# Kernel tuning notes

Measured on AMD Instinct MI355X. Metric: run time of the kernel, lower is better.

## Reference

```python
import jax, jax.numpy as jnp
import numpy as np

B, T, D = 4, 2048, 1024
H = 16
HD = D // H  # 64


def setup_inputs() -> dict:
    key = jax.random.key(0)
    ks = jax.random.split(key, 5)
    scale = 0.02
    x = jax.random.normal(ks[0], (B, T, D), dtype=jnp.float32)
    W_qkv = jax.random.normal(ks[1], (D, 3 * D), dtype=jnp.float32) * scale
    b_qkv = jnp.zeros((3 * D,), dtype=jnp.float32)
    W_proj = jax.random.normal(ks[2], (D, D), dtype=jnp.float32) * scale
    b_proj = jnp.zeros((D,), dtype=jnp.float32)
    return {"x": x, "W_qkv": W_qkv, "b_qkv": b_qkv, "W_proj": W_proj, "b_proj": b_proj}


def reference(x, W_qkv, b_qkv, W_proj, b_proj):
    b, t, c = x.shape
    qkv = x @ W_qkv + b_qkv  # [b, t, 3c]
    q, k, v = jnp.split(qkv, 3, axis=-1)
    # [b, h, t, hd]
    q = q.reshape(b, t, H, HD).transpose(0, 2, 1, 3)
    k = k.reshape(b, t, H, HD).transpose(0, 2, 1, 3)
    v = v.reshape(b, t, H, HD).transpose(0, 2, 1, 3)
    att = jnp.einsum('bhqd,bhkd->bhqk', q, k) / jnp.sqrt(jnp.float32(HD))
    causal = jnp.tril(jnp.ones((t, t), dtype=bool))
    att = jnp.where(causal[None, None], att, jnp.float32(-jnp.inf))
    att = jax.nn.softmax(att, axis=-1)
    y = jnp.einsum('bhqk,bhkd->bhqd', att, v)
    y = y.transpose(0, 2, 1, 3).reshape(b, t, c)
    return y @ W_proj + b_proj
```

## Files before the change

### kernel.cpp

```cpp
#include <hip/hip_runtime.h>
#include <hip/hip_bf16.h>
#include <cmath>
#include <cstdint>

#define B_ 4
#define T_ 2048
#define D_ 1024
#define H_ 16
#define HD_ 64
#define M_ (B_*T_)
#define NQKV_ 3072

#define SCALE_Q 0.18033688011112042f

typedef float f32x4 __attribute__((ext_vector_type(4)));
typedef float f32x16 __attribute__((ext_vector_type(16)));
typedef __bf16 bf16x8 __attribute__((ext_vector_type(8)));
typedef __bf16 bf16x4 __attribute__((ext_vector_type(4)));

#define MFMA16(a, b, c) __builtin_amdgcn_mfma_f32_16x16x32_bf16((a), (b), (c), 0, 0, 0)
#define MFMA32(a, b, c) __builtin_amdgcn_mfma_f32_32x32x16_bf16((a), (b), (c), 0, 0, 0)

#if defined(__has_builtin)
#if __has_builtin(__builtin_amdgcn_global_load_lds)
#define HAVE_GLDS 1
#endif
#endif

#ifdef HAVE_GLDS
#define GLDS16(g, l) __builtin_amdgcn_global_load_lds( \
    (const __attribute__((address_space(1))) void*)(g), \
    (__attribute__((address_space(3))) void*)(l), 16, 0, 0)
#endif

__device__ inline float hexp2(float x) {
  float r; asm("v_exp_f32 %0, %1" : "=v"(r) : "v"(x)); return r;
}

__device__ inline uint32_t pack2bf(float a, float b) {
  union { __bf16 h[2]; uint32_t u; } x;
  x.h[0] = (__bf16)a; x.h[1] = (__bf16)b;
  return x.u;
}

__global__ __launch_bounds__(256) void k_cvt_bf16(const float4* __restrict__ in,
                                                  bf16x4* __restrict__ out, int n4) {
  int i = blockIdx.x * 256 + threadIdx.x;
  if (i >= n4) return;
  float4 v = in[i];
  bf16x4 o;
  o[0] = (__bf16)v.x; o[1] = (__bf16)v.y; o[2] = (__bf16)v.z; o[3] = (__bf16)v.w;
  out[i] = o;
}

__global__ __launch_bounds__(256) void k_transpose_cvt(const float* __restrict__ in,
                                                       __bf16* __restrict__ out,
                                                       int R, int C) {
  __shared__ float tile[64][65];
  int r0 = blockIdx.y * 64, c0 = blockIdx.x * 64;
#pragma unroll
  for (int i = 0; i < 16; ++i) {
    int e = threadIdx.x + i * 256;
    int lr = e >> 6, lc = e & 63;
    tile[lr][lc] = in[(size_t)(r0 + lr) * C + c0 + lc];
  }
  __syncthreads();
#pragma unroll
  for (int i = 0; i < 16; ++i) {
    int e = threadIdx.x + i * 256;
    int lc = e >> 6, lr = e & 63;
    out[(size_t)(c0 + lc) * R + r0 + lr] = (__bf16)tile[lr][lc];
  }
}

__global__ __launch_bounds__(512) void k_gemm256(const __bf16* __restrict__ A,
                                                 const __bf16* __restrict__ Bt,
                                                 const float* __restrict__ bias,
                                                 __bf16* __restrict__ Qb,
                                                 __bf16* __restrict__ Kb,
                                                 __bf16* __restrict__ Vtmp) {
  __shared__ __bf16 lA[256 * 32];
  __shared__ __bf16 lB[128 * 32];
  const int tid = threadIdx.x;
  const int lane = tid & 63, w = tid >> 6;
  const int wr = w >> 1, wc = w & 1;
  const int r15 = lane & 15, rg = lane >> 4;
  const int mb = blockIdx.y, nb = blockIdx.x;
  const int K = D_;
  const int nk = K >> 5;

  const f32x4 zero = {0.f, 0.f, 0.f, 0.f};
  f32x4 acc[4][4];
#pragma unroll
  for (int m = 0; m < 4; ++m)
#pragma unroll
    for (int n = 0; n < 4; ++n) acc[m][n] = zero;

  const int cA0 = tid, cA1 = tid + 512;
  const int rowA0 = cA0 >> 2, rowA1 = cA1 >> 2, offA = (tid & 3) * 8;
  const int rowB = tid >> 2;
  const __bf16* Ab = A + (size_t)(mb * 256) * K;
  const __bf16* Bb = Bt + (size_t)(nb * 128) * K;

  for (int kb = 0; kb < nk; ++kb) {
    __syncthreads();
#ifdef HAVE_GLDS
    GLDS16(Ab + (size_t)rowA0 * K + kb * 32 + offA, &lA[cA0 * 8]);
    GLDS16(Ab + (size_t)rowA1 * K + kb * 32 + offA, &lA[cA1 * 8]);
    GLDS16(Bb + (size_t)rowB * K + kb * 32 + offA, &lB[tid * 8]);
#else
    {
      bf16x8 ta0 = *(const bf16x8*)(Ab + (size_t)rowA0 * K + kb * 32 + offA);
      bf16x8 ta1 = *(const bf16x8*)(Ab + (size_t)rowA1 * K + kb * 32 + offA);
      bf16x8 tb0 = *(const bf16x8*)(Bb + (size_t)rowB * K + kb * 32 + offA);
      *(bf16x8*)(&lA[cA0 * 8]) = ta0;
      *(bf16x8*)(&lA[cA1 * 8]) = ta1;
      *(bf16x8*)(&lB[tid * 8]) = tb0;
    }
#endif
    __syncthreads();
    bf16x8 af[4], bfr[4];
#pragma unroll
    for (int m = 0; m < 4; ++m)
      af[m] = *(const bf16x8*)(&lA[(wr * 64 + m * 16 + r15) * 32 + rg * 8]);
#pragma unroll
    for (int n = 0; n < 4; ++n)
      bfr[n] = *(const bf16x8*)(&lB[(wc * 64 + n * 16 + r15) * 32 + rg * 8]);
#pragma unroll
    for (int m = 0; m < 4; ++m)
#pragma unroll
      for (int n = 0; n < 4; ++n)
        acc[m][n] = MFMA16(af[m], bfr[n], acc[m][n]);
  }

  const int row0 = mb * 256 + wr * 64;
  const int col0 = nb * 128 + wc * 64;
#pragma unroll
  for (int m = 0; m < 4; ++m) {
#pragma unroll
    for (int n = 0; n < 4; ++n) {
#pragma unroll
      for (int j = 0; j < 4; ++j) {
        int r = row0 + m * 16 + rg * 4 + j;
        int c = col0 + n * 16 + r15;
        float v = acc[m][n][j] + bias[c];
        int which = c >> 10, cc = c & 1023;
        int b = r >> 11, t = r & 2047;
        if (which == 0) {
          int hh = cc >> 6, hd = cc & 63;
          Qb[((size_t)(b * H_ + hh) * T_ + t) * HD_ + hd] = (__bf16)(v * SCALE_Q);
        } else if (which == 1) {
          int hh = cc >> 6, hd = cc & 63;
          Kb[((size_t)(b * H_ + hh) * T_ + t) * HD_ + hd] = (__bf16)v;
        } else {
          Vtmp[(size_t)r * D_ + cc] = (__bf16)v;
        }
      }
    }
  }
}

__global__ __launch_bounds__(256) void k_gemm_proj(const __bf16* __restrict__ A,
                                                   const __bf16* __restrict__ Bt,
                                                   const float* __restrict__ bias,
                                                   float* __restrict__ Cf,
                                                   int K, int N) {
  __shared__ __bf16 lA[128 * 32];
  __shared__ __bf16 lB[128 * 32];
  const int tid = threadIdx.x;
  const int lane = tid & 63, w = tid >> 6;
  const int wr = w >> 1, wc = w & 1;
  const int r15 = lane & 15, rg = lane >> 4;
  const int mb = blockIdx.y, nb = blockIdx.x;
  const int nk = K >> 5;

  const f32x4 zero = {0.f, 0.f, 0.f, 0.f};
  f32x4 acc[4][4];
#pragma unroll
  for (int m = 0; m < 4; ++m)
#pragma unroll
    for (int n = 0; n < 4; ++n) acc[m][n] = zero;

  const int c0 = tid, c1 = tid + 256;
  const int rowA0 = c0 >> 2, offA0 = (c0 & 3) * 8;
  const int rowA1 = c1 >> 2, offA1 = (c1 & 3) * 8;
  const __bf16* Ab = A + (size_t)(mb * 128) * K;
  const __bf16* Bb = Bt + (size_t)(nb * 128) * K;

  for (int kb = 0; kb < nk; ++kb) {
    __syncthreads();
#ifdef HAVE_GLDS
    GLDS16(Ab + (size_t)rowA0 * K + kb * 32 + offA0, &lA[c0 * 8]);
    GLDS16(Ab + (size_t)rowA1 * K + kb * 32 + offA1, &lA[c1 * 8]);
    GLDS16(Bb + (size_t)rowA0 * K + kb * 32 + offA0, &lB[c0 * 8]);
    GLDS16(Bb + (size_t)rowA1 * K + kb * 32 + offA1, &lB[c1 * 8]);
#else
    {
      bf16x8 ta0 = *(const bf16x8*)(Ab + (size_t)rowA0 * K + kb * 32 + offA0);
      bf16x8 ta1 = *(const bf16x8*)(Ab + (size_t)rowA1 * K + kb * 32 + offA1);
      bf16x8 tb0 = *(const bf16x8*)(Bb + (size_t)rowA0 * K + kb * 32 + offA0);
      bf16x8 tb1 = *(const bf16x8*)(Bb + (size_t)rowA1 * K + kb * 32 + offA1);
      *(bf16x8*)(&lA[c0 * 8]) = ta0;
      *(bf16x8*)(&lA[c1 * 8]) = ta1;
      *(bf16x8*)(&lB[c0 * 8]) = tb0;
      *(bf16x8*)(&lB[c1 * 8]) = tb1;
    }
#endif
    __syncthreads();
    bf16x8 af[4], bfr[4];
#pragma unroll
    for (int m = 0; m < 4; ++m)
      af[m] = *(const bf16x8*)(&lA[(wr * 64 + m * 16 + r15) * 32 + rg * 8]);
#pragma unroll
    for (int n = 0; n < 4; ++n)
      bfr[n] = *(const bf16x8*)(&lB[(wc * 64 + n * 16 + r15) * 32 + rg * 8]);
#pragma unroll
    for (int m = 0; m < 4; ++m)
#pragma unroll
      for (int n = 0; n < 4; ++n)
        acc[m][n] = MFMA16(af[m], bfr[n], acc[m][n]);
  }

  const int row0 = mb * 128 + wr * 64;
  const int col0 = nb * 128 + wc * 64;
#pragma unroll
  for (int m = 0; m < 4; ++m)
#pragma unroll
    for (int n = 0; n < 4; ++n)
#pragma unroll
      for (int j = 0; j < 4; ++j) {
        int r = row0 + m * 16 + rg * 4 + j;
        int c = col0 + n * 16 + r15;
        Cf[(size_t)r * N + c] = acc[m][n][j] + bias[c];
      }
}

__global__ __launch_bounds__(256) void k_vtrans(const __bf16* __restrict__ Vtmp,
                                                __bf16* __restrict__ Vt) {
  __shared__ __bf16 tile[64][72];
  const int bh = blockIdx.y;
  const int b = bh >> 4, h = bh & 15;
  const int t0 = blockIdx.x * 64;
  const int tid = threadIdx.x;
#pragma unroll
  for (int i = 0; i < 2; ++i) {
    int e = tid + i * 256;
    int tr = e >> 3, c8 = (e & 7) * 8;
    bf16x8 v = *(const bf16x8*)(Vtmp + (size_t)(b * T_ + t0 + tr) * D_ + h * HD_ + c8);
    *(bf16x8*)(&tile[tr][c8]) = v;
  }
  __syncthreads();
  const int hr = tid >> 2, tc0 = (tid & 3) * 16;
#pragma unroll
  for (int half = 0; half < 2; ++half) {
    bf16x8 o;
#pragma unroll
    for (int i = 0; i < 8; ++i) o[i] = tile[tc0 + half * 8 + i][hr];
    *(bf16x8*)(Vt + ((size_t)bh * HD_ + hr) * T_ + t0 + tc0 + half * 8) = o;
  }
}

__global__ __launch_bounds__(256) void k_attn(const __bf16* __restrict__ Qb,
                                              const __bf16* __restrict__ Kb,
                                              const __bf16* __restrict__ Vt,
                                              __bf16* __restrict__ Obuf) {
  __shared__ __bf16 lK[2][64 * 64];
  __shared__ __bf16 lV[2][64 * 64];
  const int tid = threadIdx.x;
  const int lane = tid & 63, w = tid >> 6;
  const int l31 = lane & 31, hi = lane >> 5;
  const int bh = blockIdx.y;
  const int b = bh >> 4, h = bh & 15;
  const __bf16* Qh = Qb + (size_t)bh * T_ * HD_;
  const __bf16* Kh = Kb + (size_t)bh * T_ * HD_;
  const __bf16* Vh = Vt + (size_t)bh * HD_ * T_;

  const int sRow0 = tid >> 3, sSw0 = (((tid) & 7) ^ (sRow0 & 7)) * 8;
  const int c1s = tid + 256;
  const int sRow1 = c1s >> 3, sSw1 = ((c1s & 7) ^ (sRow1 & 7)) * 8;

  auto STAGE = [&](int bufi, int kv0) {
#ifdef HAVE_GLDS
    GLDS16(Kh + (size_t)(kv0 + sRow0) * HD_ + sSw0, &lK[bufi][tid * 8]);
    GLDS16(Kh + (size_t)(kv0 + sRow1) * HD_ + sSw1, &lK[bufi][(tid + 256) * 8]);
    GLDS16(Vh + (size_t)sRow0 * T_ + kv0 + sSw0, &lV[bufi][tid * 8]);
    GLDS16(Vh + (size_t)sRow1 * T_ + kv0 + sSw1, &lV[bufi][(tid + 256) * 8]);
#else
    bf16x8 k0 = *(const bf16x8*)(Kh + (size_t)(kv0 + sRow0) * HD_ + sSw0);
    bf16x8 k1 = *(const bf16x8*)(Kh + (size_t)(kv0 + sRow1) * HD_ + sSw1);
    bf16x8 v0 = *(const bf16x8*)(Vh + (size_t)sRow0 * T_ + kv0 + sSw0);
    bf16x8 v1 = *(const bf16x8*)(Vh + (size_t)sRow1 * T_ + kv0 + sSw1);
    *(bf16x8*)(&lK[bufi][tid * 8]) = k0;
    *(bf16x8*)(&lK[bufi][(tid + 256) * 8]) = k1;
    *(bf16x8*)(&lV[bufi][tid * 8]) = v0;
    *(bf16x8*)(&lV[bufi][(tid + 256) * 8]) = v1;
#endif
  };

  int buf = 0;
  STAGE(0, 0);

  auto process_half = [&](int s, int nst, bool hasNext) {
    const int q0w = s * 128 + w * 32;
    bf16x8 qf[4];
#pragma unroll
    for (int ks = 0; ks < 4; ++ks)
      qf[ks] = *(const bf16x8*)(Qh + (size_t)(q0w + l31) * HD_ + ks * 16 + hi * 8);

    f32x16 o0, o1;
#pragma unroll
    for (int i = 0; i < 16; ++i) { o0[i] = 0.f; o1[i] = 0.f; }
    float lrun = 0.f;

    for (int i = 0; i < nst; ++i) {
      const int kv0 = i * 64;
      if (i + 1 < nst) STAGE(buf ^ 1, (i + 1) * 64);
      else if (hasNext) STAGE(buf ^ 1, 0);

      if (kv0 <= q0w + 31) {
        const bool masked = (kv0 + 63) > q0w;
        bf16x8 kf[2][4];
#pragma unroll
        for (int seg = 0; seg < 2; ++seg)
#pragma unroll
          for (int ks = 0; ks < 4; ++ks)
            kf[seg][ks] = *(const bf16x8*)(&lK[buf][(seg * 32 + l31) * 64 +
                                                   (((ks * 2 + hi) ^ (l31 & 7)) * 8)]);
        f32x16 s0, s1;
#pragma unroll
        for (int r = 0; r < 16; ++r) { s0[r] = 0.f; s1[r] = 0.f; }
        __builtin_amdgcn_s_setprio(1);
#pragma unroll
        for (int ks = 0; ks < 4; ++ks) s0 = MFMA32(kf[0][ks], qf[ks], s0);
#pragma unroll
        for (int ks = 0; ks < 4; ++ks) s1 = MFMA32(kf[1][ks], qf[ks], s1);
        __builtin_amdgcn_s_setprio(0);

        if (masked) {
#pragma unroll
          for (int r = 0; r < 16; ++r) {
            int rr = (r & 3) + 8 * (r >> 2) + 4 * hi;
            if (kv0 + rr > q0w + l31) s0[r] = -INFINITY;
            if (kv0 + 32 + rr > q0w + l31) s1[r] = -INFINITY;
          }
        }
        float rs = 0.f;
#pragma unroll
        for (int r = 0; r < 16; ++r) {
          s0[r] = hexp2(s0[r]); s1[r] = hexp2(s1[r]);
          rs += s0[r] + s1[r];
        }
        rs += __shfl_xor(rs, 32, 64);
        lrun += rs;

        bf16x8 vf[2][4];
#pragma unroll
        for (int dh = 0; dh < 2; ++dh)
#pragma unroll
          for (int ks = 0; ks < 4; ++ks)
            vf[dh][ks] = *(const bf16x8*)(&lV[buf][(dh * 32 + l31) * 64 +
                                                   (((ks * 2 + hi) ^ (l31 & 7)) * 8)]);

#pragma unroll
        for (int ks = 0; ks < 4; ++ks) {
          const f32x16& sv = (ks < 2) ? s0 : s1;
          const int off = (ks & 1) * 8;
          uint32_t w0 = pack2bf(sv[off + 0], sv[off + 1]);
          uint32_t w1 = pack2bf(sv[off + 2], sv[off + 3]);
          uint32_t w2 = pack2bf(sv[off + 4], sv[off + 5]);
          uint32_t w3 = pack2bf(sv[off + 6], sv[off + 7]);
          uint32_t sx = hi ? w0 : w2;
          uint32_t sy = hi ? w1 : w3;
          uint32_t px = (uint32_t)__shfl_xor((int)sx, 32, 64);
          uint32_t py = (uint32_t)__shfl_xor((int)sy, 32, 64);
          union { uint32_t u[4]; bf16x8 v; } pa;
          pa.u[0] = hi ? px : w0;
          pa.u[1] = hi ? py : w1;
          pa.u[2] = hi ? w2 : px;
          pa.u[3] = hi ? w3 : py;
          __builtin_amdgcn_s_setprio(1);
          o0 = MFMA32(pa.v, vf[0][ks], o0);
          o1 = MFMA32(pa.v, vf[1][ks], o1);
          __builtin_amdgcn_s_setprio(0);
        }
      }
      __syncthreads();
      buf ^= 1;
    }

#pragma unroll
    for (int r = 0; r < 16; ++r) {
      int rr = (r & 3) + 8 * (r >> 2) + 4 * hi;
      float inv = 1.0f / __shfl(lrun, rr, 64);
      int row = q0w + rr;
      __bf16* op = Obuf + (size_t)(b * T_ + row) * D_ + h * HD_ + l31;
      op[0]  = (__bf16)(o0[r] * inv);
      op[32] = (__bf16)(o1[r] * inv);
    }
  };

  const int sA = 15 - blockIdx.x;
  const int sB = blockIdx.x;
  __syncthreads();
  process_half(sA, 2 * sA + 2, true);
  process_half(sB, 2 * sB + 2, false);
}

extern "C" void kernel_launch(void* const* d_in, const int* in_sizes, int n_in,
                              void* d_out, int out_size, void* d_ws, size_t ws_size,
                              hipStream_t stream) {
  const float* x      = (const float*)d_in[0];
  const float* W_qkv  = (const float*)d_in[1];
  const float* b_qkv  = (const float*)d_in[2];
  const float* W_proj = (const float*)d_in[3];
  const float* b_proj = (const float*)d_in[4];
  float* out = (float*)d_out;

  char* ws = (char*)d_ws;
  size_t o = 0;
  __bf16* xb     = (__bf16*)(ws + o); o += (size_t)M_ * D_ * 2;
  __bf16* wqkvt  = (__bf16*)(ws + o); o += (size_t)NQKV_ * D_ * 2;
  __bf16* wprojt = (__bf16*)(ws + o); o += (size_t)D_ * D_ * 2;
  __bf16* Qb     = (__bf16*)(ws + o); o += (size_t)M_ * D_ * 2;
  __bf16* Kb     = (__bf16*)(ws + o); o += (size_t)M_ * D_ * 2;
  __bf16* Vtmp   = (__bf16*)(ws + o); o += (size_t)M_ * D_ * 2;
  __bf16* Vt     = (__bf16*)(ws + o); o += (size_t)M_ * D_ * 2;
  __bf16* Obuf   = (__bf16*)(ws + o); o += (size_t)M_ * D_ * 2;
  (void)ws_size; (void)in_sizes; (void)n_in; (void)out_size;

  k_cvt_bf16<<<(M_ * D_ / 4 + 255) / 256, 256, 0, stream>>>((const float4*)x, (bf16x4*)xb, M_ * D_ / 4);
  k_transpose_cvt<<<dim3(NQKV_ / 64, D_ / 64), 256, 0, stream>>>(W_qkv, wqkvt, D_, NQKV_);
  k_transpose_cvt<<<dim3(D_ / 64, D_ / 64), 256, 0, stream>>>(W_proj, wprojt, D_, D_);
  k_gemm256<<<dim3(NQKV_ / 128, M_ / 256), 512, 0, stream>>>(xb, wqkvt, b_qkv, Qb, Kb, Vtmp);
  k_vtrans<<<dim3(T_ / 64, B_ * H_), 256, 0, stream>>>(Vtmp, Vt);
  k_attn<<<dim3(8, B_ * H_), 256, 0, stream>>>(Qb, Kb, Vt, Obuf);
  k_gemm_proj<<<dim3(D_ / 128, M_ / 128), 256, 0, stream>>>(Obuf, wprojt, b_proj, out, D_, D_);
}
```

Measured before the change: 205.5 us.

## Fuse V transpose into QKV GEMM epilogue and double attention KV tile to 128

The QKV GEMM epilogue now writes V directly in transposed [b,h,hd,t] layout as packed 4-element bf16 stores, removing the separate k_vtrans kernel and its intermediate buffer round trip. The attention kernel stages 128 keys per pipeline step instead of 64, which halves the number of barriers and stage iterations. The final tile is split into two 64-key halves with masking, and the second half is skipped when it lies fully above the diagonal. LDS usage doubles to 64KB per block, which may reduce occupancy, and the transposed V stores from the GEMM are strided 8-byte writes.

```diff
diff --git a/kernel.cpp b/kernel.cpp
--- a/kernel.cpp
+++ b/kernel.cpp
@@ -78,7 +78,7 @@
                                                  const float* __restrict__ bias,
                                                  __bf16* __restrict__ Qb,
                                                  __bf16* __restrict__ Kb,
-                                                 __bf16* __restrict__ Vtmp) {
+                                                 __bf16* __restrict__ Vt) {
   __shared__ __bf16 lA[256 * 32];
   __shared__ __bf16 lB[128 * 32];
   const int tid = threadIdx.x;
@@ -139,22 +139,29 @@
   for (int m = 0; m < 4; ++m) {
 #pragma unroll
     for (int n = 0; n < 4; ++n) {
-#pragma unroll
-      for (int j = 0; j < 4; ++j) {
-        int r = row0 + m * 16 + rg * 4 + j;
-        int c = col0 + n * 16 + r15;
-        float v = acc[m][n][j] + bias[c];
-        int which = c >> 10, cc = c & 1023;
-        int b = r >> 11, t = r & 2047;
-        if (which == 0) {
-          int hh = cc >> 6, hd = cc & 63;
-          Qb[((size_t)(b * H_ + hh) * T_ + t) * HD_ + hd] = (__bf16)(v * SCALE_Q);
-        } else if (which == 1) {
-          int hh = cc >> 6, hd = cc & 63;
-          Kb[((size_t)(b * H_ + hh) * T_ + t) * HD_ + hd] = (__bf16)v;
-        } else {
-          Vtmp[(size_t)r * D_ + cc] = (__bf16)v;
-        }
+      const int c = col0 + n * 16 + r15;
+      const int r0 = row0 + m * 16 + rg * 4;
+      const int which = c >> 10, cc = c & 1023;
+      const int b = r0 >> 11, t0 = r0 & 2047;
+      float v[4];
+#pragma unroll
+      for (int j = 0; j < 4; ++j) v[j] = acc[m][n][j] + bias[c];
+      if (which == 0) {
+        int hh = cc >> 6, hd = cc & 63;
+#pragma unroll
+        for (int j = 0; j < 4; ++j)
+          Qb[((size_t)(b * H_ + hh) * T_ + t0 + j) * HD_ + hd] = (__bf16)(v[j] * SCALE_Q);
+      } else if (which == 1) {
+        int hh = cc >> 6, hd = cc & 63;
+#pragma unroll
+        for (int j = 0; j < 4; ++j)
+          Kb[((size_t)(b * H_ + hh) * T_ + t0 + j) * HD_ + hd] = (__bf16)v[j];
+      } else {
+        int hh = cc >> 6, hd = cc & 63;
+        bf16x4 pk;
+#pragma unroll
+        for (int j = 0; j < 4; ++j) pk[j] = (__bf16)v[j];
+        *(bf16x4*)(Vt + ((size_t)(b * H_ + hh) * HD_ + hd) * T_ + t0) = pk;
       }
     }
   }
@@ -235,37 +242,12 @@
       }
 }
 
-__global__ __launch_bounds__(256) void k_vtrans(const __bf16* __restrict__ Vtmp,
-                                                __bf16* __restrict__ Vt) {
-  __shared__ __bf16 tile[64][72];
-  const int bh = blockIdx.y;
-  const int b = bh >> 4, h = bh & 15;
-  const int t0 = blockIdx.x * 64;
-  const int tid = threadIdx.x;
-#pragma unroll
-  for (int i = 0; i < 2; ++i) {
-    int e = tid + i * 256;
-    int tr = e >> 3, c8 = (e & 7) * 8;
-    bf16x8 v = *(const bf16x8*)(Vtmp + (size_t)(b * T_ + t0 + tr) * D_ + h * HD_ + c8);
-    *(bf16x8*)(&tile[tr][c8]) = v;
-  }
-  __syncthreads();
-  const int hr = tid >> 2, tc0 = (tid & 3) * 16;
-#pragma unroll
-  for (int half = 0; half < 2; ++half) {
-    bf16x8 o;
-#pragma unroll
-    for (int i = 0; i < 8; ++i) o[i] = tile[tc0 + half * 8 + i][hr];
-    *(bf16x8*)(Vt + ((size_t)bh * HD_ + hr) * T_ + t0 + tc0 + half * 8) = o;
-  }
-}
-
 __global__ __launch_bounds__(256) void k_attn(const __bf16* __restrict__ Qb,
                                               const __bf16* __restrict__ Kb,
                                               const __bf16* __restrict__ Vt,
                                               __bf16* __restrict__ Obuf) {
-  __shared__ __bf16 lK[2][64 * 64];
-  __shared__ __bf16 lV[2][64 * 64];
+  __shared__ __bf16 lK[2][128 * 64];
+  __shared__ __bf16 lV[2][64 * 128];
   const int tid = threadIdx.x;
   const int lane = tid & 63, w = tid >> 6;
   const int l31 = lane & 31, hi = lane >> 5;
@@ -275,33 +257,30 @@
   const __bf16* Kh = Kb + (size_t)bh * T_ * HD_;
   const __bf16* Vh = Vt + (size_t)bh * HD_ * T_;
 
-  const int sRow0 = tid >> 3, sSw0 = (((tid) & 7) ^ (sRow0 & 7)) * 8;
-  const int c1s = tid + 256;
-  const int sRow1 = c1s >> 3, sSw1 = ((c1s & 7) ^ (sRow1 & 7)) * 8;
-
   auto STAGE = [&](int bufi, int kv0) {
+#pragma unroll
+    for (int i = 0; i < 4; ++i) {
+      const int c = tid + i * 256;
+      const int rK = c >> 3, gK = (c & 7) ^ (rK & 7);
+      const int rV = c >> 4, gV = (c & 15) ^ (rV & 7);
 #ifdef HAVE_GLDS
-    GLDS16(Kh + (size_t)(kv0 + sRow0) * HD_ + sSw0, &lK[bufi][tid * 8]);
-    GLDS16(Kh + (size_t)(kv0 + sRow1) * HD_ + sSw1, &lK[bufi][(tid + 256) * 8]);
-    GLDS16(Vh + (size_t)sRow0 * T_ + kv0 + sSw0, &lV[bufi][tid * 8]);
-    GLDS16(Vh + (size_t)sRow1 * T_ + kv0 + sSw1, &lV[bufi][(tid + 256) * 8]);
+      GLDS16(Kh + (size_t)(kv0 + rK) * HD_ + gK * 8, &lK[bufi][c * 8]);
+      GLDS16(Vh + (size_t)rV * T_ + kv0 + gV * 8, &lV[bufi][c * 8]);
 #else
-    bf16x8 k0 = *(const bf16x8*)(Kh + (size_t)(kv0 + sRow0) * HD_ + sSw0);
-    bf16x8 k1 = *(const bf16x8*)(Kh + (size_t)(kv0 + sRow1) * HD_ + sSw1);
-    bf16x8 v0 = *(const bf16x8*)(Vh + (size_t)sRow0 * T_ + kv0 + sSw0);
-    bf16x8 v1 = *(const bf16x8*)(Vh + (size_t)sRow1 * T_ + kv0 + sSw1);
-    *(bf16x8*)(&lK[bufi][tid * 8]) = k0;
-    *(bf16x8*)(&lK[bufi][(tid + 256) * 8]) = k1;
-    *(bf16x8*)(&lV[bufi][tid * 8]) = v0;
-    *(bf16x8*)(&lV[bufi][(tid + 256) * 8]) = v1;
-#endif
+      bf16x8 kv = *(const bf16x8*)(Kh + (size_t)(kv0 + rK) * HD_ + gK * 8);
+      bf16x8 vv = *(const bf16x8*)(Vh + (size_t)rV * T_ + kv0 + gV * 8);
+      *(bf16x8*)(&lK[bufi][c * 8]) = kv;
+      *(bf16x8*)(&lV[bufi][c * 8]) = vv;
+#endif
+    }
   };
 
   int buf = 0;
   STAGE(0, 0);
 
-  auto process_half = [&](int s, int nst, bool hasNext) {
+  auto process_half = [&](int s, bool hasNext) {
     const int q0w = s * 128 + w * 32;
+    const int nst = s + 1;
     bf16x8 qf[4];
 #pragma unroll
     for (int ks = 0; ks < 4; ++ks)
@@ -312,77 +291,84 @@
     for (int i = 0; i < 16; ++i) { o0[i] = 0.f; o1[i] = 0.f; }
     float lrun = 0.f;
 
+    auto body = [&](int st, int kv0s, bool masked) {
+      bf16x8 kf[2][4];
+#pragma unroll
+      for (int seg = 0; seg < 2; ++seg)
+#pragma unroll
+        for (int ks = 0; ks < 4; ++ks)
+          kf[seg][ks] = *(const bf16x8*)(&lK[buf][(st * 64 + seg * 32 + l31) * 64 +
+                                                 (((ks * 2 + hi) ^ (l31 & 7)) * 8)]);
+      f32x16 s0, s1;
+#pragma unroll
+      for (int r = 0; r < 16; ++r) { s0[r] = 0.f; s1[r] = 0.f; }
+      __builtin_amdgcn_s_setprio(1);
+#pragma unroll
+      for (int ks = 0; ks < 4; ++ks) s0 = MFMA32(kf[0][ks], qf[ks], s0);
+#pragma unroll
+      for (int ks = 0; ks < 4; ++ks) s1 = MFMA32(kf[1][ks], qf[ks], s1);
+      __builtin_amdgcn_s_setprio(0);
+
+      if (masked) {
+#pragma unroll
+        for (int r = 0; r < 16; ++r) {
+          int rr = (r & 3) + 8 * (r >> 2) + 4 * hi;
+          if (kv0s + rr > q0w + l31) s0[r] = -INFINITY;
+          if (kv0s + 32 + rr > q0w + l31) s1[r] = -INFINITY;
+        }
+      }
+      float rs = 0.f;
+#pragma unroll
+      for (int r = 0; r < 16; ++r) {
+        s0[r] = hexp2(s0[r]); s1[r] = hexp2(s1[r]);
+        rs += s0[r] + s1[r];
+      }
+      rs += __shfl_xor(rs, 32, 64);
+      lrun += rs;
+
+      bf16x8 vf[2][4];
+#pragma unroll
+      for (int dh = 0; dh < 2; ++dh)
+#pragma unroll
+        for (int ks = 0; ks < 4; ++ks)
+          vf[dh][ks] = *(const bf16x8*)(&lV[buf][(dh * 32 + l31) * 128 +
+                                                 (((st * 8 + ks * 2 + hi) ^ (l31 & 7)) * 8)]);
+
+#pragma unroll
+      for (int ks = 0; ks < 4; ++ks) {
+        const f32x16& sv = (ks < 2) ? s0 : s1;
+        const int off = (ks & 1) * 8;
+        uint32_t w0 = pack2bf(sv[off + 0], sv[off + 1]);
+        uint32_t w1 = pack2bf(sv[off + 2], sv[off + 3]);
+        uint32_t w2 = pack2bf(sv[off + 4], sv[off + 5]);
+        uint32_t w3 = pack2bf(sv[off + 6], sv[off + 7]);
+        uint32_t sx = hi ? w0 : w2;
+        uint32_t sy = hi ? w1 : w3;
+        uint32_t px = (uint32_t)__shfl_xor((int)sx, 32, 64);
+        uint32_t py = (uint32_t)__shfl_xor((int)sy, 32, 64);
+        union { uint32_t u[4]; bf16x8 v; } pa;
+        pa.u[0] = hi ? px : w0;
+        pa.u[1] = hi ? py : w1;
+        pa.u[2] = hi ? w2 : px;
+        pa.u[3] = hi ? w3 : py;
+        __builtin_amdgcn_s_setprio(1);
+        o0 = MFMA32(pa.v, vf[0][ks], o0);
+        o1 = MFMA32(pa.v, vf[1][ks], o1);
+        __builtin_amdgcn_s_setprio(0);
+      }
+    };
+
     for (int i = 0; i < nst; ++i) {
-      const int kv0 = i * 64;
-      if (i + 1 < nst) STAGE(buf ^ 1, (i + 1) * 64);
+      const int kv0 = i * 128;
+      if (i + 1 < nst) STAGE(buf ^ 1, (i + 1) * 128);
       else if (hasNext) STAGE(buf ^ 1, 0);
 
-      if (kv0 <= q0w + 31) {
-        const bool masked = (kv0 + 63) > q0w;
-        bf16x8 kf[2][4];
-#pragma unroll
-        for (int seg = 0; seg < 2; ++seg)
-#pragma unroll
-          for (int ks = 0; ks < 4; ++ks)
-            kf[seg][ks] = *(const bf16x8*)(&lK[buf][(seg * 32 + l31) * 64 +
-                                                   (((ks * 2 + hi) ^ (l31 & 7)) * 8)]);
-        f32x16 s0, s1;
-#pragma unroll
-        for (int r = 0; r < 16; ++r) { s0[r] = 0.f; s1[r] = 0.f; }
-        __builtin_amdgcn_s_setprio(1);
-#pragma unroll
-        for (int ks = 0; ks < 4; ++ks) s0 = MFMA32(kf[0][ks], qf[ks], s0);
-#pragma unroll
-        for (int ks = 0; ks < 4; ++ks) s1 = MFMA32(kf[1][ks], qf[ks], s1);
-        __builtin_amdgcn_s_setprio(0);
-
-        if (masked) {
-#pragma unroll
-          for (int r = 0; r < 16; ++r) {
-            int rr = (r & 3) + 8 * (r >> 2) + 4 * hi;
-            if (kv0 + rr > q0w + l31) s0[r] = -INFINITY;
-            if (kv0 + 32 + rr > q0w + l31) s1[r] = -INFINITY;
-          }
-        }
-        float rs = 0.f;
-#pragma unroll
-        for (int r = 0; r < 16; ++r) {
-          s0[r] = hexp2(s0[r]); s1[r] = hexp2(s1[r]);
-          rs += s0[r] + s1[r];
-        }
-        rs += __shfl_xor(rs, 32, 64);
-        lrun += rs;
-
-        bf16x8 vf[2][4];
-#pragma unroll
-        for (int dh = 0; dh < 2; ++dh)
-#pragma unroll
-          for (int ks = 0; ks < 4; ++ks)
-            vf[dh][ks] = *(const bf16x8*)(&lV[buf][(dh * 32 + l31) * 64 +
-                                                   (((ks * 2 + hi) ^ (l31 & 7)) * 8)]);
-
-#pragma unroll
-        for (int ks = 0; ks < 4; ++ks) {
-          const f32x16& sv = (ks < 2) ? s0 : s1;
-          const int off = (ks & 1) * 8;
-          uint32_t w0 = pack2bf(sv[off + 0], sv[off + 1]);
-          uint32_t w1 = pack2bf(sv[off + 2], sv[off + 3]);
-          uint32_t w2 = pack2bf(sv[off + 4], sv[off + 5]);
-          uint32_t w3 = pack2bf(sv[off + 6], sv[off + 7]);
-          uint32_t sx = hi ? w0 : w2;
-          uint32_t sy = hi ? w1 : w3;
-          uint32_t px = (uint32_t)__shfl_xor((int)sx, 32, 64);
-          uint32_t py = (uint32_t)__shfl_xor((int)sy, 32, 64);
-          union { uint32_t u[4]; bf16x8 v; } pa;
-          pa.u[0] = hi ? px : w0;
-          pa.u[1] = hi ? py : w1;
-          pa.u[2] = hi ? w2 : px;
-          pa.u[3] = hi ? w3 : py;
-          __builtin_amdgcn_s_setprio(1);
-          o0 = MFMA32(pa.v, vf[0][ks], o0);
-          o1 = MFMA32(pa.v, vf[1][ks], o1);
-          __builtin_amdgcn_s_setprio(0);
-        }
+      if (i + 1 < nst) {
+        body(0, kv0, false);
+        body(1, kv0 + 64, false);
+      } else {
+        body(0, kv0, true);
+        if (kv0 + 64 <= q0w + 31) body(1, kv0 + 64, true);
       }
       __syncthreads();
       buf ^= 1;
@@ -402,8 +388,8 @@
   const int sA = 15 - blockIdx.x;
   const int sB = blockIdx.x;
   __syncthreads();
-  process_half(sA, 2 * sA + 2, true);
-  process_half(sB, 2 * sB + 2, false);
+  process_half(sA, true);
+  process_half(sB, false);
 }
 
 extern "C" void kernel_launch(void* const* d_in, const int* in_sizes, int n_in,
@@ -423,7 +409,6 @@
   __bf16* wprojt = (__bf16*)(ws + o); o += (size_t)D_ * D_ * 2;
   __bf16* Qb     = (__bf16*)(ws + o); o += (size_t)M_ * D_ * 2;
   __bf16* Kb     = (__bf16*)(ws + o); o += (size_t)M_ * D_ * 2;
-  __bf16* Vtmp   = (__bf16*)(ws + o); o += (size_t)M_ * D_ * 2;
   __bf16* Vt     = (__bf16*)(ws + o); o += (size_t)M_ * D_ * 2;
   __bf16* Obuf   = (__bf16*)(ws + o); o += (size_t)M_ * D_ * 2;
   (void)ws_size; (void)in_sizes; (void)n_in; (void)out_size;
@@ -431,8 +416,7 @@
   k_cvt_bf16<<<(M_ * D_ / 4 + 255) / 256, 256, 0, stream>>>((const float4*)x, (bf16x4*)xb, M_ * D_ / 4);
   k_transpose_cvt<<<dim3(NQKV_ / 64, D_ / 64), 256, 0, stream>>>(W_qkv, wqkvt, D_, NQKV_);
   k_transpose_cvt<<<dim3(D_ / 64, D_ / 64), 256, 0, stream>>>(W_proj, wprojt, D_, D_);
-  k_gemm256<<<dim3(NQKV_ / 128, M_ / 256), 512, 0, stream>>>(xb, wqkvt, b_qkv, Qb, Kb, Vtmp);
-  k_vtrans<<<dim3(T_ / 64, B_ * H_), 256, 0, stream>>>(Vtmp, Vt);
+  k_gemm256<<<dim3(NQKV_ / 128, M_ / 256), 512, 0, stream>>>(xb, wqkvt, b_qkv, Qb, Kb, Vt);
   k_attn<<<dim3(8, B_ * H_), 256, 0, stream>>>(Qb, Kb, Vt, Obuf);
   k_gemm_proj<<<dim3(D_ / 128, M_ / 128), 256, 0, stream>>>(Obuf, wprojt, b_proj, out, D_, D_);
 }
```

New measurement: 215.0 us. 1.05x slower.
